# Performance work log

Hardware: AMD Instinct MI355X
Metric: run time of the kernel (lower is better)

The kernel has to match this reference:

```python
import jax, jax.numpy as jnp
import numpy as np

B, S, D = 2, 1024, 1024
N_HEADS = 16
R = 128
M = 8
N_NEURONS = 256


def group_gate(gate, n_basis):
    # gate: [B,S,N] -> [B,S,M], sum over consecutive groups, then normalize
    b, s, n = gate.shape
    gs = n // n_basis  # exact by construction (256/8)
    g = gate.reshape(b, s, n_basis, gs).sum(axis=-1)
    return g / (g.sum(axis=-1, keepdims=True) + 1e-8)


def feature_fn(x, neurons, weights):
    # x:[B,S,D], neurons:[M,D,R], weights:[B,S,M] -> h:[B,S,R]
    all_h = jnp.einsum('bsd,mdr->bsmr', x, neurons)
    return jnp.einsum('bsmr,bsm->bsr', all_h, weights)


def restore_fn(h, neurons, weights):
    # h:[B,S,R], neurons:[M,R,D], weights:[B,S,M] -> [B,S,D]
    pre = jnp.einsum('bsr,bsm->bsmr', h, weights)
    return jnp.einsum('bsmr,mrd->bsd', pre, neurons)


def setup_inputs() -> dict:
    key = jax.random.key(0)
    ks = jax.random.split(key, 9)
    sc = 0.02
    return {
        'x': jax.random.normal(ks[0], (B, S, D), jnp.float32),
        'qk_f': jax.random.normal(ks[1], (M, D, R), jnp.float32) * sc,
        'qk_r': jax.random.normal(ks[2], (M, R, D), jnp.float32) * sc,
        'v_f': jax.random.normal(ks[3], (M, D, R), jnp.float32) * sc,
        'v_r': jax.random.normal(ks[4], (M, R, D), jnp.float32) * sc,
        'Wg_q': jax.random.normal(ks[5], (D, N_NEURONS), jnp.float32) * sc,
        'Wg_k': jax.random.normal(ks[6], (D, N_NEURONS), jnp.float32) * sc,
        'Wg_v': jax.random.normal(ks[7], (D, N_NEURONS), jnp.float32) * sc,
        'W_O': jax.random.normal(ks[8], (D, D), jnp.float32) * sc,
    }


def reference(x, qk_f, qk_r, v_f, v_r, Wg_q, Wg_k, Wg_v, W_O):
    # Router gates (softmax over neuron dim), then grouped per basis
    g_Q = jax.nn.softmax(jnp.einsum('bsd,dn->bsn', x, Wg_q), axis=-1)
    g_K = jax.nn.softmax(jnp.einsum('bsd,dn->bsn', x, Wg_k), axis=-1)
    g_V = jax.nn.softmax(jnp.einsum('bsd,dn->bsn', x, Wg_v), axis=-1)
    gQ_b = group_gate(g_Q, M)
    gK_b = group_gate(g_K, M)
    gV_b = group_gate(g_V, M)

    Q = restore_fn(feature_fn(x, qk_f, gQ_b), qk_r, gQ_b)
    K = restore_fn(feature_fn(x, qk_f, gK_b), qk_r, gK_b)
    V = restore_fn(feature_fn(x, v_f, gV_b), v_r, gV_b)

    d_head = D // N_HEADS
    Q = Q.reshape(B, S, N_HEADS, d_head).transpose(0, 2, 1, 3)
    K = K.reshape(B, S, N_HEADS, d_head).transpose(0, 2, 1, 3)
    V = V.reshape(B, S, N_HEADS, d_head).transpose(0, 2, 1, 3)

    scale = jnp.sqrt(jnp.float32(d_head))
    scores = jnp.einsum('bhsd,bhtd->bhst', Q, K) / scale
    causal = jnp.tril(jnp.ones((S, S), dtype=jnp.bool_))
    scores = jnp.where(causal, scores, jnp.finfo(scores.dtype).min)
    attn_w = jax.nn.softmax(scores, axis=-1)
    out = jnp.einsum('bhst,bhtd->bhsd', attn_w, V)
    out = out.transpose(0, 2, 1, 3).reshape(B, S, D)
    out = jnp.einsum('bsd,de->bse', out, W_O)
    return out
```

## Files before the change

### kernel.cpp

```cpp
#include <hip/hip_runtime.h>
#include <hip/hip_bf16.h>

#define BB 2
#define SS 1024
#define DD 1024
#define NH 16
#define DH 64
#define MM 8
#define RR 128
#define NN 256
#define NT (BB*SS)

using bf16 = __hip_bfloat16;

typedef __attribute__((ext_vector_type(8))) short short8;
typedef __attribute__((ext_vector_type(4))) short short4v;
typedef __attribute__((ext_vector_type(4))) float f32x4;

#define EXP2F(x) __builtin_amdgcn_exp2f(x)

#define GLD16(g, l) __builtin_amdgcn_global_load_lds( \
    (const __attribute__((address_space(1))) void*)(g), \
    (__attribute__((address_space(3))) void*)(l), 16, 0, 0)

__device__ __forceinline__ short8 lds_load8(const short* p) {
    short4v a = *(const short4v*)p;
    short4v b = *(const short4v*)(p + 4);
    short8 r;
    r[0] = a[0]; r[1] = a[1]; r[2] = a[2]; r[3] = a[3];
    r[4] = b[0]; r[5] = b[1]; r[6] = b[2]; r[7] = b[3];
    return r;
}

template <int NR>
__device__ __forceinline__ void stage_tile(const bf16* __restrict__ src, int k0,
                                           bf16* lds, int wave, int lane) {
#pragma unroll
    for (int i = 0; i < NR / 32; ++i) {
        const int L = i * 256 + wave * 64 + lane;
        const int row = L >> 3;
        const int gch = (L & 7) ^ ((row >> 1) & 7);
        GLD16(src + (size_t)row * DD + k0 + gch * 8, &lds[(i * 256 + wave * 64) * 8]);
    }
}

__device__ __forceinline__ short8 fragld(const bf16* lds, int rc, int kk, int quad) {
    int slot = (kk * 4 + quad) ^ ((rc >> 1) & 7);
    return *(const short8*)&((const short*)lds)[(rc * 8 + slot) * 8];
}

__device__ __forceinline__ void gemm64_pipe(
    const bf16* __restrict__ A, const bf16* __restrict__ Bt, bf16* __restrict__ C,
    int Nz, int m0, int n0, bf16* As, bf16* Bs,
    int wave, int lane, int quad, int l15) {
    const int wr = wave >> 1, wc = wave & 1;
    f32x4 acc[2][4];
#pragma unroll
    for (int i = 0; i < 2; ++i)
#pragma unroll
        for (int j = 0; j < 4; ++j) acc[i][j] = (f32x4)0.f;

    const bf16* Ab = A + (size_t)m0 * DD;
    const bf16* Bb = Bt + (size_t)n0 * DD;

    stage_tile<64>(Ab, 0, As, wave, lane);
    stage_tile<128>(Bb, 0, Bs, wave, lane);
    __syncthreads();

    for (int k0 = 0; k0 < DD; k0 += 64) {
        const int buf = (k0 >> 6) & 1;
        const bf16* Asc = As + buf * (64 * 64);
        const bf16* Bsc = Bs + buf * (128 * 64);
        if (k0 + 64 < DD) {
            stage_tile<64>(Ab, k0 + 64, As + (buf ^ 1) * (64 * 64), wave, lane);
            stage_tile<128>(Bb, k0 + 64, Bs + (buf ^ 1) * (128 * 64), wave, lane);
        }
#pragma unroll
        for (int kk = 0; kk < 2; ++kk) {
            short8 aF[2], bF[4];
#pragma unroll
            for (int bi = 0; bi < 2; ++bi) aF[bi] = fragld(Asc, wr * 32 + bi * 16 + l15, kk, quad);
#pragma unroll
            for (int bj = 0; bj < 4; ++bj) bF[bj] = fragld(Bsc, wc * 64 + bj * 16 + l15, kk, quad);
#pragma unroll
            for (int bi = 0; bi < 2; ++bi)
#pragma unroll
                for (int bj = 0; bj < 4; ++bj)
                    acc[bi][bj] = __builtin_amdgcn_mfma_f32_16x16x32_bf16(aF[bi], bF[bj], acc[bi][bj], 0, 0, 0);
        }
        __syncthreads();
    }

#pragma unroll
    for (int bi = 0; bi < 2; ++bi)
#pragma unroll
        for (int bj = 0; bj < 4; ++bj)
#pragma unroll
            for (int r = 0; r < 4; ++r) {
                int row = m0 + wr * 32 + bi * 16 + quad * 4 + r;
                int col = n0 + wc * 64 + bj * 16 + l15;
                C[(size_t)row * Nz + col] = __float2bfloat16(acc[bi][bj][r]);
            }
}

struct ProjArgs {
    const bf16 *xb, *f0, *f1, *wg;
    bf16 *allh0, *allh1, *lg;
    const float* csrc[3];
    bf16* cdst[3];
};

__global__ __launch_bounds__(256, 3) void mfma_proj(ProjArgs P) {
    __shared__ __align__(16) char smem[49152];
    const int bidx = blockIdx.x;
    const int tid = threadIdx.x;

    if (bidx >= 704) {
        float (*tile)[33] = (float(*)[33])smem;
        const int cb = bidx - 704;
        const int j = cb >> 10;
        const int t = cb & 1023;
        const int kb = t >> 5, rb = t & 31;
        const int tx = tid & 31, ty0 = tid >> 5;
        const float* s = P.csrc[j] + ((size_t)(kb * 32) * 1024) + rb * 32 + tx;
#pragma unroll
        for (int p = 0; p < 4; ++p)
            tile[ty0 + p * 8][tx] = s[(size_t)(ty0 + p * 8) * 1024];
        __syncthreads();
        bf16* dd = P.cdst[j] + ((size_t)(rb * 32) * 1024) + kb * 32 + tx;
#pragma unroll
        for (int p = 0; p < 4; ++p)
            dd[(size_t)(ty0 + p * 8) * 1024] = __float2bfloat16(tile[tx][ty0 + p * 8]);
        return;
    }

    bf16* As = (bf16*)smem;
    bf16* Bs = As + 2 * 64 * 64;
    const int wave = tid >> 6, lane = tid & 63;
    const int quad = lane >> 4, l15 = lane & 15;
    const int wk = (bidx & 7) * 88 + (bidx >> 3);
    if (wk < 512) {
        const int z = wk >> 8;
        const int r = wk & 255;
        gemm64_pipe(P.xb, z ? P.f1 : P.f0, z ? P.allh1 : P.allh0, 1024,
                    (r >> 3) * 64, (r & 7) * 128, As, Bs, wave, lane, quad, l15);
    } else {
        const int r = wk - 512;
        gemm64_pipe(P.xb, P.wg, P.lg, 768, (r / 6) * 64, (r % 6) * 128,
                    As, Bs, wave, lane, quad, l15);
    }
}

struct RestZ {
    const bf16* A[3];
    const bf16* Bt[3];
    bf16* C[3];
};

__global__ __launch_bounds__(256, 3) void mfma_restore(RestZ R) {
    __shared__ __align__(16) char smem[49152];
    bf16* As = (bf16*)smem;
    bf16* Bs = As + 2 * 64 * 64;
    const int tid = threadIdx.x;
    const int wave = tid >> 6, lane = tid & 63;
    const int quad = lane >> 4, l15 = lane & 15;
    const int wk = (blockIdx.x & 7) * 96 + (blockIdx.x >> 3);
    const int z = wk >> 8;
    const int r = wk & 255;
    gemm64_pipe(R.A[z], R.Bt[z], R.C[z], DD, (r >> 3) * 64, (r & 7) * 128,
                As, Bs, wave, lane, quad, l15);
}

__global__ __launch_bounds__(256, 4) void mfma_wo(
    const bf16* __restrict__ A, const bf16* __restrict__ Bt, float* __restrict__ C) {
    __shared__ __align__(16) bf16 As[2 * 64 * 64];
    __shared__ __align__(16) bf16 Bs[2 * 64 * 64];
    const int tid = threadIdx.x;
    const int wave = tid >> 6, lane = tid & 63;
    const int quad = lane >> 4, l15 = lane & 15;
    const int wr = wave >> 1, wc = wave & 1;
    const int wk = (blockIdx.x & 7) * 64 + (blockIdx.x >> 3);
    const int m0 = (wk >> 4) * 64, n0 = (wk & 15) * 64;

    f32x4 acc[2][2];
#pragma unroll
    for (int i = 0; i < 2; ++i)
#pragma unroll
        for (int j = 0; j < 2; ++j) acc[i][j] = (f32x4)0.f;

    const bf16* Ab = A + (size_t)m0 * DD;
    const bf16* Bb = Bt + (size_t)n0 * DD;

    stage_tile<64>(Ab, 0, As, wave, lane);
    stage_tile<64>(Bb, 0, Bs, wave, lane);
    __syncthreads();

    for (int k0 = 0; k0 < DD; k0 += 64) {
        const int buf = (k0 >> 6) & 1;
        const bf16* Asc = As + buf * (64 * 64);
        const bf16* Bsc = Bs + buf * (64 * 64);
        if (k0 + 64 < DD) {
            stage_tile<64>(Ab, k0 + 64, As + (buf ^ 1) * (64 * 64), wave, lane);
            stage_tile<64>(Bb, k0 + 64, Bs + (buf ^ 1) * (64 * 64), wave, lane);
        }
#pragma unroll
        for (int kk = 0; kk < 2; ++kk) {
            short8 aF[2], bF[2];
#pragma unroll
            for (int bi = 0; bi < 2; ++bi) aF[bi] = fragld(Asc, wr * 32 + bi * 16 + l15, kk, quad);
#pragma unroll
            for (int bj = 0; bj < 2; ++bj) bF[bj] = fragld(Bsc, wc * 32 + bj * 16 + l15, kk, quad);
#pragma unroll
            for (int bi = 0; bi < 2; ++bi)
#pragma unroll
                for (int bj = 0; bj < 2; ++bj)
                    acc[bi][bj] = __builtin_amdgcn_mfma_f32_16x16x32_bf16(aF[bi], bF[bj], acc[bi][bj], 0, 0, 0);
        }
        __syncthreads();
    }
#pragma unroll
    for (int bi = 0; bi < 2; ++bi)
#pragma unroll
        for (int bj = 0; bj < 2; ++bj)
#pragma unroll
            for (int r = 0; r < 4; ++r) {
                int row = m0 + wr * 32 + bi * 16 + quad * 4 + r;
                int col = n0 + wc * 32 + bj * 16 + l15;
                C[(size_t)row * DD + col] = acc[bi][bj][r];
            }
}

struct ConvJobs {
    const float* src[9];
    bf16* dst[9];
    int K[9], R[9], G[9];
    int tEnd[9];
};

__global__ void convert_kernel(ConvJobs J) {
    __shared__ float tile[32][33];
    const int b = blockIdx.x;
    int j = 0;
    while (j < 8 && b >= J.tEnd[j]) ++j;
    const int local = b - (j > 0 ? J.tEnd[j - 1] : 0);
    const float* src = J.src[j];
    bf16* dst = J.dst[j];
    const int tid = threadIdx.x;

    if (J.G[j] == 0) {
        size_t base = (size_t)local * 4096 + (size_t)tid * 16;
        const float4* s4 = (const float4*)(src + base);
        short* d = (short*)(dst + base);
#pragma unroll
        for (int c = 0; c < 4; ++c) {
            float4 v = s4[c];
            short4v o;
            bf16 t0 = __float2bfloat16(v.x); o[0] = *(short*)&t0;
            bf16 t1 = __float2bfloat16(v.y); o[1] = *(short*)&t1;
            bf16 t2 = __float2bfloat16(v.z); o[2] = *(short*)&t2;
            bf16 t3 = __float2bfloat16(v.w); o[3] = *(short*)&t3;
            *(short4v*)(d + c * 4) = o;
        }
    } else {
        const int Kj = J.K[j], Rj = J.R[j];
        const int Rb = Rj >> 5, Kb = Kj >> 5;
        const int perG = Kb * Rb;
        const int g = local / perG;
        const int rem = local - g * perG;
        const int kb = rem / Rb, rb = rem - kb * Rb;
        const int tx = tid & 31, ty0 = tid >> 5;
        const float* s = src + ((size_t)(g * Kj + kb * 32) * Rj) + rb * 32 + tx;
#pragma unroll
        for (int p = 0; p < 4; ++p)
            tile[ty0 + p * 8][tx] = s[(size_t)(ty0 + p * 8) * Rj];
        __syncthreads();
        bf16* dd = dst + ((size_t)(g * Rj + rb * 32) * Kj) + kb * 32 + tx;
#pragma unroll
        for (int p = 0; p < 4; ++p)
            dd[(size_t)(ty0 + p * 8) * Kj] = __float2bfloat16(tile[tx][ty0 + p * 8]);
    }
}

__global__ void gate_combine(const bf16* __restrict__ logitsAll,
                             const bf16* __restrict__ allh,
                             bf16* __restrict__ preQ, bf16* __restrict__ preK,
                             bf16* __restrict__ preV) {
    const int t = blockIdx.x;
    const int n = threadIdx.x;
    const int wave = n >> 6, lane = n & 63;
    __shared__ float wred[3][4];
    __shared__ float sred[3][4];
    __shared__ float gred[3][8];

    float v[3], e[3];
#pragma unroll
    for (int z = 0; z < 3; ++z)
        v[z] = __bfloat162float(logitsAll[(size_t)t * 768 + z * 256 + n]);

    float mz[3];
#pragma unroll
    for (int z = 0; z < 3; ++z) {
        mz[z] = v[z];
#pragma unroll
        for (int off = 1; off <= 32; off <<= 1)
            mz[z] = fmaxf(mz[z], __shfl_xor(mz[z], off));
    }
    if (lane == 0) {
#pragma unroll
        for (int z = 0; z < 3; ++z) wred[z][wave] = mz[z];
    }
    __syncthreads();
    float gmax[3];
#pragma unroll
    for (int z = 0; z < 3; ++z)
        gmax[z] = fmaxf(fmaxf(wred[z][0], wred[z][1]), fmaxf(wred[z][2], wred[z][3]));

    float ws[3];
#pragma unroll
    for (int z = 0; z < 3; ++z) {
        e[z] = __expf(v[z] - gmax[z]);
        ws[z] = e[z];
#pragma unroll
        for (int off = 1; off <= 32; off <<= 1)
            ws[z] += __shfl_xor(ws[z], off);
    }
    if (lane == 0) {
#pragma unroll
        for (int z = 0; z < 3; ++z) sred[z][wave] = ws[z];
    }
    float gs[3];
#pragma unroll
    for (int z = 0; z < 3; ++z) {
        gs[z] = e[z];
#pragma unroll
        for (int off = 1; off <= 16; off <<= 1)
            gs[z] += __shfl_xor(gs[z], off);
    }
    __syncthreads();
    float total[3];
#pragma unroll
    for (int z = 0; z < 3; ++z)
        total[z] = sred[z][0] + sred[z][1] + sred[z][2] + sred[z][3];
    if ((n & 31) == 0) {
#pragma unroll
        for (int z = 0; z < 3; ++z) gred[z][n >> 5] = gs[z] / total[z];
    }
    __syncthreads();

    float gv[3][8];
#pragma unroll
    for (int z = 0; z < 3; ++z) {
        float tot = 0.f;
#pragma unroll
        for (int m = 0; m < 8; ++m) tot += gred[z][m];
        float inv = 1.0f / (tot + 1e-8f);
#pragma unroll
        for (int m = 0; m < 8; ++m) gv[z][m] = gred[z][m] * inv;
    }

    const int r0 = n & 127;
    const int half = n >> 7;
    const bf16* src_qk = allh + (size_t)t * 1024;
    const bf16* src_v  = allh + (size_t)NT * DD + (size_t)t * 1024;
    float hq = 0.f, hk = 0.f, hv = 0.f;
#pragma unroll
    for (int m = 0; m < 8; ++m) {
        float aqk = __bfloat162float(src_qk[m * 128 + r0]);
        float av  = __bfloat162float(src_v[m * 128 + r0]);
        hq += aqk * gv[0][m];
        hk += aqk * gv[1][m];
        hv += av  * gv[2][m];
    }
    __syncthreads();
#pragma unroll
    for (int mm = 0; mm < 4; ++mm) {
        int m = half * 4 + mm;
        size_t o = (size_t)t * 1024 + m * 128 + r0;
        preQ[o] = __float2bfloat16(hq * gv[0][m]);
        preK[o] = __float2bfloat16(hk * gv[1][m]);
        preV[o] = __float2bfloat16(hv * gv[2][m]);
    }
}

#define LDK 68

__global__ __launch_bounds__(256) void flash_attn_causal(
    const bf16* __restrict__ Q, const bf16* __restrict__ K,
    const bf16* __restrict__ V, bf16* __restrict__ out) {
    const int bx = blockIdx.x;
    const int xcd = bx & 7, slot = bx >> 3;
    const int bh = xcd * 4 + (slot & 3);
    const int qtk = slot >> 2;
    const int qt = (qtk < 8) ? (15 - qtk) : (qtk - 8);
    const int b = bh >> 4;
    const int h = bh & 15;
    const int kt_hi = qt + 1;

    const int tid = threadIdx.x;
    const int wave = tid >> 6;
    const int lane = tid & 63;
    const int quad = lane >> 4;
    const int l15 = lane & 15;

    __shared__ short Ks[2][64 * 64];
    __shared__ short Vt[2][64 * LDK];
    __shared__ short Ps[4 * 16 * LDK];

    const int q_row = qt * 64 + wave * 16 + l15;
    const bf16* qptr = Q + (size_t)(b * SS + q_row) * DD + h * DH + quad * 8;
    short8 aq0 = *(const short8*)qptr;
    short8 aq1 = *(const short8*)(qptr + 32);

    const int krp = tid & 31;
    const int dhb = (tid >> 5) * 8;

    float m_r[4], l_r[4];
    f32x4 o[4];
#pragma unroll
    for (int r = 0; r < 4; ++r) { m_r[r] = -3.0e38f; l_r[r] = 0.f; }
#pragma unroll
    for (int cc = 0; cc < 4; ++cc) o[cc] = (f32x4)0.f;

    const float SCL2 = 0.18033688f;

    {
#pragma unroll
        for (int i = 0; i < 2; ++i) {
            const int L = i * 256 + wave * 64 + lane;
            const int row = L >> 3;
            const int gch = (L & 7) ^ ((row >> 1) & 7);
            GLD16(K + (size_t)(b * SS + row) * DD + h * DH + gch * 8,
                  &Ks[0][(i * 256 + wave * 64) * 8]);
        }
        const bf16* s0 = V + (size_t)(b * SS + 2 * krp) * DD + h * DH + dhb;
        short8 r0 = *(const short8*)s0;
        short8 r1 = *(const short8*)(s0 + DD);
#pragma unroll
        for (int i = 0; i < 8; ++i) {
            unsigned int pk = (unsigned short)r0[i] | ((unsigned int)(unsigned short)r1[i] << 16);
            *(unsigned int*)&Vt[0][(dhb + i) * LDK + 2 * krp] = pk;
        }
        __syncthreads();
    }

    for (int kt = 0; kt < kt_hi; ++kt) {
        const int buf = kt & 1;
        const bool pf = (kt + 1 < kt_hi);
        short8 pr0, pr1;
        if (pf) {
#pragma unroll
            for (int i = 0; i < 2; ++i) {
                const int L = i * 256 + wave * 64 + lane;
                const int row = L >> 3;
                const int gch = (L & 7) ^ ((row >> 1) & 7);
                GLD16(K + (size_t)(b * SS + (kt + 1) * 64 + row) * DD + h * DH + gch * 8,
                      &Ks[buf ^ 1][(i * 256 + wave * 64) * 8]);
            }
            const bf16* s0 = V + (size_t)(b * SS + (kt + 1) * 64 + 2 * krp) * DD + h * DH + dhb;
            pr0 = *(const short8*)s0;
            pr1 = *(const short8*)(s0 + DD);
        }

        const short* KsB = Ks[buf];
        f32x4 s[4];
#pragma unroll
        for (int cc = 0; cc < 4; ++cc) {
            int n = cc * 16 + l15;
            int sl0 = quad ^ ((n >> 1) & 7);
            int sl1 = (quad + 4) ^ ((n >> 1) & 7);
            short8 bk0 = *(const short8*)&KsB[(n * 8 + sl0) * 8];
            short8 bk1 = *(const short8*)&KsB[(n * 8 + sl1) * 8];
            f32x4 acc = (f32x4)0.f;
            acc = __builtin_amdgcn_mfma_f32_16x16x32_bf16(aq0, bk0, acc, 0, 0, 0);
            acc = __builtin_amdgcn_mfma_f32_16x16x32_bf16(aq1, bk1, acc, 0, 0, 0);
            s[cc] = acc;
        }

        const bool diag = (kt == qt);
#pragma unroll
        for (int cc = 0; cc < 4; ++cc) {
#pragma unroll
            for (int r = 0; r < 4; ++r) {
                float v = s[cc][r] * SCL2;
                if (diag) {
                    int row_rel = wave * 16 + quad * 4 + r;
                    int col_rel = cc * 16 + l15;
                    if (col_rel > row_rel) v = -3.0e38f;
                }
                s[cc][r] = v;
            }
        }

        float mx[4];
#pragma unroll
        for (int r = 0; r < 4; ++r) {
            float m2 = fmaxf(fmaxf(s[0][r], s[1][r]), fmaxf(s[2][r], s[3][r]));
            m2 = fmaxf(m2, __shfl_xor(m2, 1));
            m2 = fmaxf(m2, __shfl_xor(m2, 2));
            m2 = fmaxf(m2, __shfl_xor(m2, 4));
            m2 = fmaxf(m2, __shfl_xor(m2, 8));
            mx[r] = m2;
        }
        bool grew = false;
#pragma unroll
        for (int r = 0; r < 4; ++r) grew = grew || (mx[r] > m_r[r] + 8.f);
        float alpha[4];
        const bool need = __any(grew);
        if (need) {
#pragma unroll
            for (int r = 0; r < 4; ++r) {
                float nm = fmaxf(m_r[r], mx[r]);
                alpha[r] = EXP2F(m_r[r] - nm);
                m_r[r] = nm;
            }
        }

        float p[4][4];
#pragma unroll
        for (int r = 0; r < 4; ++r) {
            float rs = 0.f;
#pragma unroll
            for (int cc = 0; cc < 4; ++cc) {
                float e = EXP2F(s[cc][r] - m_r[r]);
                p[cc][r] = e;
                rs += e;
            }
            rs += __shfl_xor(rs, 1);
            rs += __shfl_xor(rs, 2);
            rs += __shfl_xor(rs, 4);
            rs += __shfl_xor(rs, 8);
            if (need) l_r[r] = l_r[r] * alpha[r] + rs;
            else      l_r[r] += rs;
        }
        if (need) {
#pragma unroll
            for (int cc = 0; cc < 4; ++cc)
#pragma unroll
                for (int r = 0; r < 4; ++r) o[cc][r] *= alpha[r];
        }

        short* pw = &Ps[wave * 16 * LDK];
#pragma unroll
        for (int cc = 0; cc < 4; ++cc)
#pragma unroll
            for (int r = 0; r < 4; ++r) {
                bf16 hb = __float2bfloat16(p[cc][r]);
                pw[(quad * 4 + r) * LDK + cc * 16 + l15] = *(short*)&hb;
            }

        short8 ap0 = lds_load8(&pw[l15 * LDK + quad * 8]);
        short8 ap1 = lds_load8(&pw[l15 * LDK + 32 + quad * 8]);

        const short* VtB = Vt[buf];
#pragma unroll
        for (int cc = 0; cc < 4; ++cc) {
            short8 bv0 = lds_load8(&VtB[(cc * 16 + l15) * LDK + quad * 8]);
            short8 bv1 = lds_load8(&VtB[(cc * 16 + l15) * LDK + 32 + quad * 8]);
            o[cc] = __builtin_amdgcn_mfma_f32_16x16x32_bf16(ap0, bv0, o[cc], 0, 0, 0);
            o[cc] = __builtin_amdgcn_mfma_f32_16x16x32_bf16(ap1, bv1, o[cc], 0, 0, 0);
        }

        if (pf) {
#pragma unroll
            for (int i = 0; i < 8; ++i) {
                unsigned int pk = (unsigned short)pr0[i] | ((unsigned int)(unsigned short)pr1[i] << 16);
                *(unsigned int*)&Vt[buf ^ 1][(dhb + i) * LDK + 2 * krp] = pk;
            }
        }
        __syncthreads();
    }

    float inv[4];
#pragma unroll
    for (int r = 0; r < 4; ++r) inv[r] = 1.0f / l_r[r];
#pragma unroll
    for (int cc = 0; cc < 4; ++cc)
#pragma unroll
        for (int r = 0; r < 4; ++r) {
            int row = qt * 64 + wave * 16 + quad * 4 + r;
            out[(size_t)(b * SS + row) * DD + h * DH + cc * 16 + l15] =
                __float2bfloat16(o[cc][r] * inv[r]);
        }
}

extern "C" void kernel_launch(void* const* d_in, const int* in_sizes, int n_in,
                              void* d_out, int out_size, void* d_ws, size_t ws_size,
                              hipStream_t stream) {
    const float* x    = (const float*)d_in[0];
    const float* qk_f = (const float*)d_in[1];
    const float* qk_r = (const float*)d_in[2];
    const float* v_f  = (const float*)d_in[3];
    const float* v_r  = (const float*)d_in[4];
    const float* Wg_q = (const float*)d_in[5];
    const float* Wg_k = (const float*)d_in[6];
    const float* Wg_v = (const float*)d_in[7];
    const float* W_O  = (const float*)d_in[8];

    char* w = (char*)d_ws;
    const size_t MB = 1 << 20;
    bf16* xb     = (bf16*)(w + 0);
    bf16* wg_bt  = (bf16*)(w + 4 * MB);
    bf16* fbt    = (bf16*)(w + (size_t)(5.5 * MB));
    bf16* logits = (bf16*)(w + (size_t)(9.5 * MB));
    bf16* qkr_bt = (bf16*)(w + 16 * MB);
    bf16* vr_bt  = (bf16*)(w + 18 * MB);
    bf16* wo_bt  = (bf16*)(w + 20 * MB);
    bf16* preQ   = (bf16*)(w + 0);
    bf16* preK   = (bf16*)(w + 4 * MB);
    bf16* Kb     = (bf16*)(w + 8 * MB);
    bf16* Vb     = (bf16*)(w + 12 * MB);
    bf16* attnb  = (bf16*)(w + 0);
    bf16* allh   = (bf16*)d_out;
    bf16* preV   = allh + (size_t)NT * DD;
    bf16* Qb     = (bf16*)d_out;
    float* out   = (float*)d_out;

    ConvJobs J;
    J.src[0] = x;    J.dst[0] = xb;               J.K[0] = 0;    J.R[0] = 0;    J.G[0] = 0;
    J.src[1] = qk_f; J.dst[1] = fbt;              J.K[1] = 1024; J.R[1] = 128;  J.G[1] = 8;
    J.src[2] = v_f;  J.dst[2] = fbt + 1024*1024;  J.K[2] = 1024; J.R[2] = 128;  J.G[2] = 8;
    J.src[3] = Wg_q; J.dst[3] = wg_bt;            J.K[3] = 1024; J.R[3] = 256;  J.G[3] = 1;
    J.src[4] = Wg_k; J.dst[4] = wg_bt + 256*1024; J.K[4] = 1024; J.R[4] = 256;  J.G[4] = 1;
    J.src[5] = Wg_v; J.dst[5] = wg_bt + 2*256*1024; J.K[5] = 1024; J.R[5] = 256; J.G[5] = 1;
    int tiles[6] = {512, 1024, 1024, 256, 256, 256};
    int cum = 0;
    for (int i = 0; i < 6; ++i) { cum += tiles[i]; J.tEnd[i] = cum; }
    for (int i = 6; i < 9; ++i) { J.tEnd[i] = cum; J.src[i] = nullptr; J.dst[i] = nullptr; J.K[i] = J.R[i] = J.G[i] = 0; }
    convert_kernel<<<cum, 256, 0, stream>>>(J);

    ProjArgs Pp;
    Pp.xb = xb; Pp.f0 = fbt; Pp.f1 = fbt + 1024*1024; Pp.wg = wg_bt;
    Pp.allh0 = allh; Pp.allh1 = allh + (size_t)NT * DD; Pp.lg = logits;
    Pp.csrc[0] = qk_r; Pp.csrc[1] = v_r; Pp.csrc[2] = W_O;
    Pp.cdst[0] = qkr_bt; Pp.cdst[1] = vr_bt; Pp.cdst[2] = wo_bt;
    mfma_proj<<<dim3(3776), 256, 0, stream>>>(Pp);

    gate_combine<<<NT, 256, 0, stream>>>(logits, allh, preQ, preK, preV);

    RestZ Pr;
    Pr.A[0] = preQ; Pr.A[1] = preK; Pr.A[2] = preV;
    Pr.Bt[0] = qkr_bt; Pr.Bt[1] = qkr_bt; Pr.Bt[2] = vr_bt;
    Pr.C[0] = Qb; Pr.C[1] = Kb; Pr.C[2] = Vb;
    mfma_restore<<<dim3(768), 256, 0, stream>>>(Pr);

    flash_attn_causal<<<dim3(512), 256, 0, stream>>>(Qb, Kb, Vb, attnb);

    mfma_wo<<<dim3(512), 256, 0, stream>>>(attnb, wo_bt, out);
}
```

Measured before the change: 186.7 us.

## Triple-buffer LDS staging in projection, restore and output GEMMs

Changes the three MFMA GEMM kernels from double- to triple-buffered LDS staging with a prefetch distance of two k-tiles. Explicit vmcnt waits replace the full __syncthreads, so two global-to-LDS loads can stay in flight while the current tile is computed. Shared memory per block rises (73.7KB for proj/restore), which lowers the launch-bound occupancy from 3 to 2 blocks, or 4 to 3 for W_O. That trades fewer resident waves for deeper memory latency hiding.

```diff
diff --git a/kernel.cpp b/kernel.cpp
--- a/kernel.cpp
+++ b/kernel.cpp
@@ -49,7 +49,7 @@
     return *(const short8*)&((const short*)lds)[(rc * 8 + slot) * 8];
 }
 
-__device__ __forceinline__ void gemm64_pipe(
+__device__ __forceinline__ void gemm64_pipe2(
     const bf16* __restrict__ A, const bf16* __restrict__ Bt, bf16* __restrict__ C,
     int Nz, int m0, int n0, bf16* As, bf16* Bs,
     int wave, int lane, int quad, int l15) {
@@ -65,16 +65,26 @@
 
     stage_tile<64>(Ab, 0, As, wave, lane);
     stage_tile<128>(Bb, 0, Bs, wave, lane);
-    __syncthreads();
-
-    for (int k0 = 0; k0 < DD; k0 += 64) {
-        const int buf = (k0 >> 6) & 1;
-        const bf16* Asc = As + buf * (64 * 64);
-        const bf16* Bsc = Bs + buf * (128 * 64);
-        if (k0 + 64 < DD) {
-            stage_tile<64>(Ab, k0 + 64, As + (buf ^ 1) * (64 * 64), wave, lane);
-            stage_tile<128>(Bb, k0 + 64, Bs + (buf ^ 1) * (128 * 64), wave, lane);
-        }
+    stage_tile<64>(Ab, 64, As + 4096, wave, lane);
+    stage_tile<128>(Bb, 64, Bs + 8192, wave, lane);
+
+    int cur = 0;
+    for (int it = 0; it < 16; ++it) {
+        const int k0 = it * 64;
+        int nxt = cur + 2; if (nxt >= 3) nxt -= 3;
+        if (it < 14) {
+            stage_tile<64>(Ab, k0 + 128, As + nxt * 4096, wave, lane);
+            stage_tile<128>(Bb, k0 + 128, Bs + nxt * 8192, wave, lane);
+            asm volatile("s_waitcnt vmcnt(12)" ::: "memory");
+        } else if (it == 14) {
+            asm volatile("s_waitcnt vmcnt(6)" ::: "memory");
+        } else {
+            asm volatile("s_waitcnt vmcnt(0)" ::: "memory");
+        }
+        __builtin_amdgcn_s_barrier();
+
+        const bf16* Asc = As + cur * 4096;
+        const bf16* Bsc = Bs + cur * 8192;
 #pragma unroll
         for (int kk = 0; kk < 2; ++kk) {
             short8 aF[2], bF[4];
@@ -88,7 +98,8 @@
                 for (int bj = 0; bj < 4; ++bj)
                     acc[bi][bj] = __builtin_amdgcn_mfma_f32_16x16x32_bf16(aF[bi], bF[bj], acc[bi][bj], 0, 0, 0);
         }
-        __syncthreads();
+        __builtin_amdgcn_s_barrier();
+        cur = cur + 1; if (cur == 3) cur = 0;
     }
 
 #pragma unroll
@@ -110,8 +121,8 @@
     bf16* cdst[3];
 };
 
-__global__ __launch_bounds__(256, 3) void mfma_proj(ProjArgs P) {
-    __shared__ __align__(16) char smem[49152];
+__global__ __launch_bounds__(256, 2) void mfma_proj(ProjArgs P) {
+    __shared__ __align__(16) char smem[73728];
     const int bidx = blockIdx.x;
     const int tid = threadIdx.x;
 
@@ -135,19 +146,19 @@
     }
 
     bf16* As = (bf16*)smem;
-    bf16* Bs = As + 2 * 64 * 64;
+    bf16* Bs = As + 3 * 64 * 64;
     const int wave = tid >> 6, lane = tid & 63;
     const int quad = lane >> 4, l15 = lane & 15;
     const int wk = (bidx & 7) * 88 + (bidx >> 3);
     if (wk < 512) {
         const int z = wk >> 8;
         const int r = wk & 255;
-        gemm64_pipe(P.xb, z ? P.f1 : P.f0, z ? P.allh1 : P.allh0, 1024,
-                    (r >> 3) * 64, (r & 7) * 128, As, Bs, wave, lane, quad, l15);
+        gemm64_pipe2(P.xb, z ? P.f1 : P.f0, z ? P.allh1 : P.allh0, 1024,
+                     (r >> 3) * 64, (r & 7) * 128, As, Bs, wave, lane, quad, l15);
     } else {
         const int r = wk - 512;
-        gemm64_pipe(P.xb, P.wg, P.lg, 768, (r / 6) * 64, (r % 6) * 128,
-                    As, Bs, wave, lane, quad, l15);
+        gemm64_pipe2(P.xb, P.wg, P.lg, 768, (r / 6) * 64, (r % 6) * 128,
+                     As, Bs, wave, lane, quad, l15);
     }
 }
 
@@ -157,24 +168,24 @@
     bf16* C[3];
 };
 
-__global__ __launch_bounds__(256, 3) void mfma_restore(RestZ R) {
-    __shared__ __align__(16) char smem[49152];
+__global__ __launch_bounds__(256, 2) void mfma_restore(RestZ R) {
+    __shared__ __align__(16) char smem[73728];
     bf16* As = (bf16*)smem;
-    bf16* Bs = As + 2 * 64 * 64;
+    bf16* Bs = As + 3 * 64 * 64;
     const int tid = threadIdx.x;
     const int wave = tid >> 6, lane = tid & 63;
     const int quad = lane >> 4, l15 = lane & 15;
     const int wk = (blockIdx.x & 7) * 96 + (blockIdx.x >> 3);
     const int z = wk >> 8;
     const int r = wk & 255;
-    gemm64_pipe(R.A[z], R.Bt[z], R.C[z], DD, (r >> 3) * 64, (r & 7) * 128,
-                As, Bs, wave, lane, quad, l15);
-}
-
-__global__ __launch_bounds__(256, 4) void mfma_wo(
+    gemm64_pipe2(R.A[z], R.Bt[z], R.C[z], DD, (r >> 3) * 64, (r & 7) * 128,
+                 As, Bs, wave, lane, quad, l15);
+}
+
+__global__ __launch_bounds__(256, 3) void mfma_wo(
     const bf16* __restrict__ A, const bf16* __restrict__ Bt, float* __restrict__ C) {
-    __shared__ __align__(16) bf16 As[2 * 64 * 64];
-    __shared__ __align__(16) bf16 Bs[2 * 64 * 64];
+    __shared__ __align__(16) bf16 As[3 * 64 * 64];
+    __shared__ __align__(16) bf16 Bs[3 * 64 * 64];
     const int tid = threadIdx.x;
     const int wave = tid >> 6, lane = tid & 63;
     const int quad = lane >> 4, l15 = lane & 15;
@@ -193,16 +204,26 @@
 
     stage_tile<64>(Ab, 0, As, wave, lane);
     stage_tile<64>(Bb, 0, Bs, wave, lane);
-    __syncthreads();
-
-    for (int k0 = 0; k0 < DD; k0 += 64) {
-        const int buf = (k0 >> 6) & 1;
-        const bf16* Asc = As + buf * (64 * 64);
-        const bf16* Bsc = Bs + buf * (64 * 64);
-        if (k0 + 64 < DD) {
-            stage_tile<64>(Ab, k0 + 64, As + (buf ^ 1) * (64 * 64), wave, lane);
-            stage_tile<64>(Bb, k0 + 64, Bs + (buf ^ 1) * (64 * 64), wave, lane);
-        }
+    stage_tile<64>(Ab, 64, As + 4096, wave, lane);
+    stage_tile<64>(Bb, 64, Bs + 4096, wave, lane);
+
+    int cur = 0;
+    for (int it = 0; it < 16; ++it) {
+        const int k0 = it * 64;
+        int nxt = cur + 2; if (nxt >= 3) nxt -= 3;
+        if (it < 14) {
+            stage_tile<64>(Ab, k0 + 128, As + nxt * 4096, wave, lane);
+            stage_tile<64>(Bb, k0 + 128, Bs + nxt * 4096, wave, lane);
+            asm volatile("s_waitcnt vmcnt(8)" ::: "memory");
+        } else if (it == 14) {
+            asm volatile("s_waitcnt vmcnt(4)" ::: "memory");
+        } else {
+            asm volatile("s_waitcnt vmcnt(0)" ::: "memory");
+        }
+        __builtin_amdgcn_s_barrier();
+
+        const bf16* Asc = As + cur * 4096;
+        const bf16* Bsc = Bs + cur * 4096;
 #pragma unroll
         for (int kk = 0; kk < 2; ++kk) {
             short8 aF[2], bF[2];
@@ -216,7 +237,8 @@
                 for (int bj = 0; bj < 2; ++bj)
                     acc[bi][bj] = __builtin_amdgcn_mfma_f32_16x16x32_bf16(aF[bi], bF[bj], acc[bi][bj], 0, 0, 0);
         }
-        __syncthreads();
+        __builtin_amdgcn_s_barrier();
+        cur = cur + 1; if (cur == 3) cur = 0;
     }
 #pragma unroll
     for (int bi = 0; bi < 2; ++bi)
```

Result: no change. 183.0 us (-2.0%).
